# Kernel optimization log

Hardware: AMD Instinct MI355X
Metric: run time of the kernel (lower is better)

Reference implementation:

```python
import jax, jax.numpy as jnp
import numpy as np

B, S, D, H = 4, 2048, 1024, 16
DEPTH = D // H


def setup_inputs() -> dict:
    key = jax.random.key(0)
    ks = jax.random.split(key, 12)
    inp = {
        "Q": jax.random.normal(ks[0], (B, S, D), jnp.float32),
        "K": jax.random.normal(ks[1], (B, S, D), jnp.float32),
        "V": jax.random.normal(ks[2], (B, S, D), jnp.float32),
        "mask": jax.random.randint(ks[3], (B, 1, S, S), 0, 2, jnp.int32),
        "Wq": jax.random.normal(ks[4], (D, D), jnp.float32) / np.sqrt(D),
        "bq": jnp.zeros((D,), jnp.float32),
        "Wk": jax.random.normal(ks[5], (D, D), jnp.float32) / np.sqrt(D),
        "bk": jnp.zeros((D,), jnp.float32),
        "Wv": jax.random.normal(ks[6], (D, D), jnp.float32) / np.sqrt(D),
        "bv": jnp.zeros((D,), jnp.float32),
        "Wo": jax.random.normal(ks[7], (D, D), jnp.float32) / np.sqrt(D),
        "bo": jnp.zeros((D,), jnp.float32),
    }
    return inp


def _split_heads(x):
    # (B, S, D) -> (B, H, S, depth)
    b, s, _ = x.shape
    return x.reshape(b, s, H, DEPTH).transpose(0, 2, 1, 3)


def reference(Q, K, V, mask, Wq, bq, Wk, bk, Wv, bv, Wo, bo):
    q = _split_heads(Q @ Wq + bq)  # (B,H,S,d)
    k = _split_heads(K @ Wk + bk)
    v = _split_heads(V @ Wv + bv)
    scores = jnp.einsum("bhqd,bhkd->bhqk", q, k) / jnp.sqrt(jnp.float32(DEPTH))
    m = mask.astype(jnp.bool_).astype(jnp.float32)  # (B,1,S,S)
    scores = scores + (1.0 - m) * -1e9
    attn = jax.nn.softmax(scores, axis=-1)  # (B,H,S,S)
    ctx = jnp.einsum("bhqk,bhkd->bhqd", attn, v)
    ctx = ctx.transpose(0, 2, 1, 3).reshape(Q.shape[0], -1, D)  # (B,S,D)
    out = ctx @ Wo + bo
    return out, attn
```

## Files before the change

kernel.cpp:

```cpp
#include <hip/hip_runtime.h>
#include <hip/hip_bf16.h>

#define B_ 4
#define S_ 2048
#define D_ 1024
#define H_ 16
#define TSZ 8388608L

typedef short short8 __attribute__((ext_vector_type(8)));
typedef float f32x4 __attribute__((ext_vector_type(4)));

__device__ inline unsigned short f2b(float f) {
  __hip_bfloat16 h = __float2bfloat16(f);
  return __builtin_bit_cast(unsigned short, h);
}
__device__ inline void gld16(const unsigned short* g, unsigned short* l) {
  __builtin_amdgcn_global_load_lds(
      (const __attribute__((address_space(1))) void*)g,
      (__attribute__((address_space(3))) void*)l, 16, 0, 0);
}

__global__ __launch_bounds__(256) void mask_pack(const int* __restrict__ mask,
                                                 unsigned int* __restrict__ mp) {
  long t = (long)blockIdx.x * 256 + threadIdx.x;
  const int4* p = (const int4*)(mask + (t >> 4) * (long)S_ + (t & 15) * 128);
  unsigned int w0 = 0, w1 = 0, w2 = 0, w3 = 0;
#pragma unroll
  for (int c = 0; c < 32; c++) {
    int4 v = p[c];
#pragma unroll
    for (int e = 0; e < 4; e++) {
      int k = c * 4 + e;
      int val = e == 0 ? v.x : e == 1 ? v.y : e == 2 ? v.z : v.w;
      int nb = k >> 4, p16 = k & 15;
      int gg = p16 >> 2, r = p16 & 3;
      unsigned bit = ((unsigned)val & 1u) << (nb * 4 + r);
      if (gg == 0) w0 |= bit; else if (gg == 1) w1 |= bit;
      else if (gg == 2) w2 |= bit; else w3 |= bit;
    }
  }
  *(uint4*)(mp + t * 4) = make_uint4(w0, w1, w2, w3);
}

__global__ __launch_bounds__(256) void cvt3(
    const float* __restrict__ Q, const float* __restrict__ K,
    const float* __restrict__ V, unsigned short* __restrict__ qo,
    unsigned short* __restrict__ ko, unsigned short* __restrict__ vo) {
  int seg = blockIdx.x >> 12;
  long i = ((long)(blockIdx.x & 4095) * 256 + threadIdx.x) * 8;
  const float* in = seg == 0 ? Q : seg == 1 ? K : V;
  unsigned short* out = seg == 0 ? qo : seg == 1 ? ko : vo;
  float4 a = *(const float4*)(in + i);
  float4 b = *(const float4*)(in + i + 4);
  short8 u;
  u[0] = (short)f2b(a.x); u[1] = (short)f2b(a.y);
  u[2] = (short)f2b(a.z); u[3] = (short)f2b(a.w);
  u[4] = (short)f2b(b.x); u[5] = (short)f2b(b.y);
  u[6] = (short)f2b(b.z); u[7] = (short)f2b(b.w);
  *(short8*)(out + i) = u;
}

__global__ __launch_bounds__(256) void transpose_w4(
    const float* __restrict__ W0, const float* __restrict__ W1,
    const float* __restrict__ W2, const float* __restrict__ W3,
    unsigned short* __restrict__ T0, unsigned short* __restrict__ T1,
    unsigned short* __restrict__ T2, unsigned short* __restrict__ T3) {
  __shared__ unsigned short t[64 * 72];
  const int z = blockIdx.z;
  const float* W = z == 0 ? W0 : z == 1 ? W1 : z == 2 ? W2 : W3;
  unsigned short* Wt = z == 0 ? T0 : z == 1 ? T1 : z == 2 ? T2 : T3;
  const int tid = threadIdx.x;
  const int k0 = blockIdx.x * 64, n0 = blockIdx.y * 64;
#pragma unroll
  for (int p = 0; p < 4; p++) {
    int e = (p * 256 + tid) * 4;
    int r = e >> 6, c = e & 63;
    float4 v = *(const float4*)(W + (long)(k0 + r) * D_ + n0 + c);
    ushort4 u;
    u.x = f2b(v.x); u.y = f2b(v.y); u.z = f2b(v.z); u.w = f2b(v.w);
    *(ushort4*)(&t[r * 72 + c]) = u;
  }
  __syncthreads();
#pragma unroll
  for (int p = 0; p < 2; p++) {
    int e = (p * 256 + tid) * 8;
    int n = e >> 6, kc = e & 63;
    short8 x;
#pragma unroll
    for (int i = 0; i < 8; i++) x[i] = (short)t[(kc + i) * 72 + n];
    *(short8*)(Wt + (long)(n0 + n) * D_ + k0 + kc) = x;
  }
}

__global__ __launch_bounds__(256) void qkv_gemm(
    const unsigned short* __restrict__ qa, const unsigned short* __restrict__ ka,
    const unsigned short* __restrict__ va, const unsigned short* __restrict__ wq,
    const unsigned short* __restrict__ wk, const unsigned short* __restrict__ wv,
    const float* __restrict__ bqp, const float* __restrict__ bkp,
    const float* __restrict__ bvp, unsigned short* __restrict__ qo,
    unsigned short* __restrict__ ko, unsigned short* __restrict__ vo) {
  __shared__ unsigned short Asm[128 * 32];
  __shared__ unsigned short Bsm[128 * 32];
  const int z = blockIdx.z;
  const unsigned short* A = z == 0 ? qa : z == 1 ? ka : va;
  const unsigned short* Wt = z == 0 ? wq : z == 1 ? wk : wv;
  const float* bias = z == 0 ? bqp : z == 1 ? bkp : bvp;
  unsigned short* outp = z == 0 ? qo : z == 1 ? ko : vo;
  const int tid = threadIdx.x;
  const int lane = tid & 63, wid = tid >> 6;
  const int g = lane >> 4, li = lane & 15;
  const int wm = wid >> 1, wn = wid & 1;
  const long bm = (long)blockIdx.x * 128;
  const long bn = (long)blockIdx.y * 128;

  f32x4 acc[4][4];
#pragma unroll
  for (int i = 0; i < 4; i++)
#pragma unroll
    for (int j = 0; j < 4; j++) acc[i][j] = (f32x4){0.f, 0.f, 0.f, 0.f};

  for (int kt = 0; kt < 32; ++kt) {
    const int k0 = kt * 32;
    __syncthreads();
#pragma unroll
    for (int p = 0; p < 2; p++) {
      int ci = p * 256 + wid * 64 + lane;
      int r = ci >> 2, c = (ci & 3) * 8;
      gld16(A + (bm + r) * 1024L + k0 + c, &Asm[(p * 256 + wid * 64) * 8]);
      gld16(Wt + (bn + r) * 1024L + k0 + c, &Bsm[(p * 256 + wid * 64) * 8]);
    }
    __syncthreads();
    short8 af[4], bf[4];
#pragma unroll
    for (int i = 0; i < 4; i++)
      af[i] = *(const short8*)(&Asm[(wm * 64 + i * 16 + li) * 32 + g * 8]);
#pragma unroll
    for (int i = 0; i < 4; i++)
      bf[i] = *(const short8*)(&Bsm[(wn * 64 + i * 16 + li) * 32 + g * 8]);
#pragma unroll
    for (int i = 0; i < 4; i++)
#pragma unroll
      for (int j = 0; j < 4; j++)
        acc[i][j] =
            __builtin_amdgcn_mfma_f32_16x16x32_bf16(af[i], bf[j], acc[i][j], 0, 0, 0);
  }

#pragma unroll
  for (int i = 0; i < 4; i++) {
    int row0 = (int)bm + wm * 64 + i * 16 + g * 4;
#pragma unroll
    for (int j = 0; j < 4; j++) {
      int col = (int)bn + wn * 64 + j * 16 + li;
      float bvv = bias[col];
      if (z == 2) {
        int b = row0 >> 11, s0 = row0 & 2047;
        int h = col >> 6, dd = col & 63;
        ushort4 u;
#pragma unroll
        for (int jj = 0; jj < 4; jj++) u[jj] = f2b(acc[i][j][jj] + bvv);
        *(ushort4*)(outp + ((long)(b * H_ + h) * 64 + dd) * S_ + s0) = u;
      } else {
#pragma unroll
        for (int jj = 0; jj < 4; jj++) {
          int row = row0 + jj;
          int b = row >> 11, s = row & 2047;
          int h = col >> 6, dd = col & 63;
          outp[(((long)(b * H_ + h)) * S_ + s) * 64 + dd] =
              f2b(acc[i][j][jj] + bvv);
        }
      }
    }
  }
}

__global__ __launch_bounds__(256) void wo_gemm(
    const unsigned short* __restrict__ A, const unsigned short* __restrict__ Wt,
    const float* __restrict__ bias, float* __restrict__ out) {
  __shared__ unsigned short Asm[128 * 32];
  __shared__ unsigned short Bsm[128 * 32];
  const int tid = threadIdx.x;
  const int lane = tid & 63, wid = tid >> 6;
  const int g = lane >> 4, li = lane & 15;
  const int wm = wid >> 1, wn = wid & 1;
  const long bm = (long)blockIdx.x * 128;
  const long bn = (long)blockIdx.y * 128;

  f32x4 acc[4][4];
#pragma unroll
  for (int i = 0; i < 4; i++)
#pragma unroll
    for (int j = 0; j < 4; j++) acc[i][j] = (f32x4){0.f, 0.f, 0.f, 0.f};

  for (int kt = 0; kt < 32; ++kt) {
    const int k0 = kt * 32;
    __syncthreads();
#pragma unroll
    for (int p = 0; p < 2; p++) {
      int ci = p * 256 + wid * 64 + lane;
      int r = ci >> 2, c = (ci & 3) * 8;
      gld16(A + (bm + r) * 1024L + k0 + c, &Asm[(p * 256 + wid * 64) * 8]);
      gld16(Wt + (bn + r) * 1024L + k0 + c, &Bsm[(p * 256 + wid * 64) * 8]);
    }
    __syncthreads();
    short8 af[4], bf[4];
#pragma unroll
    for (int i = 0; i < 4; i++)
      af[i] = *(const short8*)(&Asm[(wm * 64 + i * 16 + li) * 32 + g * 8]);
#pragma unroll
    for (int i = 0; i < 4; i++)
      bf[i] = *(const short8*)(&Bsm[(wn * 64 + i * 16 + li) * 32 + g * 8]);
#pragma unroll
    for (int i = 0; i < 4; i++)
#pragma unroll
      for (int j = 0; j < 4; j++)
        acc[i][j] =
            __builtin_amdgcn_mfma_f32_16x16x32_bf16(af[i], bf[j], acc[i][j], 0, 0, 0);
  }

#pragma unroll
  for (int i = 0; i < 4; i++) {
    int row0 = (int)bm + wm * 64 + i * 16 + g * 4;
#pragma unroll
    for (int j = 0; j < 4; j++) {
      int col = (int)bn + wn * 64 + j * 16 + li;
      float bvv = bias[col];
#pragma unroll
      for (int jj = 0; jj < 4; jj++)
        out[(long)(row0 + jj) * 1024 + col] = acc[i][j][jj] + bvv;
    }
  }
}

__global__ __launch_bounds__(256, 4) void attn_kernel(
    const unsigned short* __restrict__ q,
    const unsigned short* __restrict__ k,
    const unsigned short* __restrict__ vt,
    const unsigned int* __restrict__ mpk,
    float* __restrict__ attn,
    unsigned short* __restrict__ ctx) {
  __shared__ unsigned short k_lds[128 * 72];
  __shared__ unsigned short vt_lds[64 * 136];
  const int tid = threadIdx.x;
  const int lane = tid & 63, wid = tid >> 6;
  const int g = lane >> 4, li = lane & 15;
  const int p0 = blockIdx.x + 32 * blockIdx.y;
  const int xcd = p0 & 7, q8 = p0 >> 3;
  const int bx = q8 & 31;
  const int bh = xcd * 8 + (q8 >> 5);
  const int b = bh >> 4, h = bh & 15;
  const int qw = bx * 64 + wid * 16;
  const int qs = qw + li;

  const unsigned short* qp = q + ((long)bh * S_ + qw) * 64;
  const short8 aq0 = *(const short8*)(qp + li * 64 + g * 8);
  const short8 aq1 = *(const short8*)(qp + li * 64 + 32 + g * 8);
  const unsigned int* mp = mpk + (((long)b * S_ + qs) * 16) * 4 + g;

  const unsigned short* kbase = k + (long)bh * S_ * 64;
  const unsigned short* vbase = vt + (long)bh * 64 * S_;
  int kst[4], kgo[4], vst[4], vgo[4];
#pragma unroll
  for (int p = 0; p < 4; p++) {
    int e = (p * 256 + tid) * 8;
    int krr = e >> 6, kcc = e & 63;
    kst[p] = krr * 72 + kcc;
    kgo[p] = krr * 64 + kcc;
    int vrr = e >> 7, vcc = e & 127;
    int c0 = ((vcc >> 5) << 5) + ((vcc & 8) << 1) + ((vcc & 16) >> 2);
    vst[p] = vrr * 136 + c0;
    vgo[p] = vrr * S_ + vcc;
  }

  float lsum = 0.f;
  short8 kreg[4];
#pragma unroll
  for (int p = 0; p < 4; p++)
    kreg[p] = *(const short8*)(kbase + kgo[p]);
  unsigned int mb_n = mp[0];
  for (int kt = 0; kt < 16; ++kt) {
    __syncthreads();
#pragma unroll
    for (int p = 0; p < 4; p++)
      *(short8*)(&k_lds[kst[p]]) = kreg[p];
    unsigned int mb = mb_n;
    if (kt < 15) {
#pragma unroll
      for (int p = 0; p < 4; p++)
        kreg[p] = *(const short8*)(kbase + (kt + 1) * 8192 + kgo[p]);
      mb_n = mp[(kt + 1) * 4];
    }
    __syncthreads();
#pragma unroll
    for (int nb = 0; nb < 8; nb++) {
      short8 b0 = *(const short8*)(&k_lds[(nb * 16 + li) * 72 + g * 8]);
      short8 b1 = *(const short8*)(&k_lds[(nb * 16 + li) * 72 + 32 + g * 8]);
      f32x4 s = (f32x4){0.f, 0.f, 0.f, 0.f};
      __builtin_amdgcn_s_setprio(1);
      s = __builtin_amdgcn_mfma_f32_16x16x32_bf16(b0, aq0, s, 0, 0, 0);
      s = __builtin_amdgcn_mfma_f32_16x16x32_bf16(b1, aq1, s, 0, 0, 0);
      __builtin_amdgcn_s_setprio(0);
#pragma unroll
      for (int r = 0; r < 4; r++) {
        float sc = s[r] * 0.125f + (((mb >> (nb * 4 + r)) & 1u) ? 0.f : -1e9f);
        lsum += __expf(sc);
      }
    }
  }
  lsum += __shfl_xor(lsum, 16);
  lsum += __shfl_xor(lsum, 32);
  const float linv = (lsum > 0.f) ? 1.0f / lsum : 0.f;

  f32x4 c[4];
#pragma unroll
  for (int i = 0; i < 4; i++) c[i] = (f32x4){0.f, 0.f, 0.f, 0.f};

  short8 vreg[4];
#pragma unroll
  for (int p = 0; p < 4; p++) {
    kreg[p] = *(const short8*)(kbase + kgo[p]);
    vreg[p] = *(const short8*)(vbase + vgo[p]);
  }
  mb_n = mp[0];
  for (int kt = 0; kt < 16; ++kt) {
    __syncthreads();
#pragma unroll
    for (int p = 0; p < 4; p++) {
      *(short8*)(&k_lds[kst[p]]) = kreg[p];
      ushort4* vh = (ushort4*)&vreg[p];
      *(ushort4*)(&vt_lds[vst[p]]) = vh[0];
      *(ushort4*)(&vt_lds[vst[p] + 8]) = vh[1];
    }
    unsigned int mb = mb_n;
    if (kt < 15) {
#pragma unroll
      for (int p = 0; p < 4; p++) {
        kreg[p] = *(const short8*)(kbase + (kt + 1) * 8192 + kgo[p]);
        vreg[p] = *(const short8*)(vbase + (kt + 1) * 128 + vgo[p]);
      }
      mb_n = mp[(kt + 1) * 4];
    }
    __syncthreads();
    float* arow = attn + ((long)bh * S_ + qs) * S_ + kt * 128;
    short8 pu2[4];
#pragma unroll
    for (int nb = 0; nb < 8; nb++) {
      short8 b0 = *(const short8*)(&k_lds[(nb * 16 + li) * 72 + g * 8]);
      short8 b1 = *(const short8*)(&k_lds[(nb * 16 + li) * 72 + 32 + g * 8]);
      f32x4 s = (f32x4){0.f, 0.f, 0.f, 0.f};
      __builtin_amdgcn_s_setprio(1);
      s = __builtin_amdgcn_mfma_f32_16x16x32_bf16(b0, aq0, s, 0, 0, 0);
      s = __builtin_amdgcn_mfma_f32_16x16x32_bf16(b1, aq1, s, 0, 0, 0);
      __builtin_amdgcn_s_setprio(0);
      f32x4 pf;
      ushort4 pu;
#pragma unroll
      for (int r = 0; r < 4; r++) {
        float sc = s[r] * 0.125f + (((mb >> (nb * 4 + r)) & 1u) ? 0.f : -1e9f);
        float pv = __expf(sc) * linv;
        pf[r] = pv;
        pu[r] = f2b(pv);
      }
      __builtin_nontemporal_store(pf, (f32x4*)(arow + nb * 16 + g * 4));
      ((ushort4*)&pu2[nb >> 1])[nb & 1] = pu;
    }
    __builtin_amdgcn_s_setprio(1);
#pragma unroll
    for (int kc = 0; kc < 4; kc++) {
      short8 ap = pu2[kc];
#pragma unroll
      for (int nb2 = 0; nb2 < 4; nb2++) {
        short8 bv =
            *(const short8*)(&vt_lds[(nb2 * 16 + li) * 136 + kc * 32 + g * 8]);
        c[nb2] = __builtin_amdgcn_mfma_f32_16x16x32_bf16(ap, bv, c[nb2], 0, 0, 0);
      }
    }
    __builtin_amdgcn_s_setprio(0);
  }

#pragma unroll
  for (int nb2 = 0; nb2 < 4; nb2++) {
#pragma unroll
    for (int j = 0; j < 4; j++) {
      int qrow = qw + g * 4 + j;
      ctx[((long)(b * S_ + qrow)) * D_ + h * 64 + nb2 * 16 + li] = f2b(c[nb2][j]);
    }
  }
}

extern "C" void kernel_launch(void* const* d_in, const int* in_sizes, int n_in,
                              void* d_out, int out_size, void* d_ws, size_t ws_size,
                              hipStream_t stream) {
  const float* Q = (const float*)d_in[0];
  const float* K = (const float*)d_in[1];
  const float* V = (const float*)d_in[2];
  const int* mask = (const int*)d_in[3];
  const float* Wq = (const float*)d_in[4];
  const float* bq = (const float*)d_in[5];
  const float* Wk = (const float*)d_in[6];
  const float* bk = (const float*)d_in[7];
  const float* Wv = (const float*)d_in[8];
  const float* bv = (const float*)d_in[9];
  const float* Wo = (const float*)d_in[10];
  const float* bo = (const float*)d_in[11];

  float* out = (float*)d_out;
  float* attn = out + TSZ;
  unsigned int* mpack = (unsigned int*)d_out;

  unsigned short* ws = (unsigned short*)d_ws;
  unsigned short* qh = ws;
  unsigned short* kh = ws + TSZ;
  unsigned short* vt = ws + 2 * TSZ;
  unsigned short* ctx = ws + 3 * TSZ;
  unsigned short* qbf = ws + 4 * TSZ;
  unsigned short* kbf = ws + 5 * TSZ;
  unsigned short* vbf = ws + 6 * TSZ;
  unsigned short* wtq = ws + 7 * TSZ;
  unsigned short* wtk = wtq + 1048576;
  unsigned short* wtv = wtk + 1048576;
  unsigned short* wto = wtv + 1048576;

  dim3 bb(256);
  mask_pack<<<512, bb, 0, stream>>>(mask, mpack);
  cvt3<<<12288, bb, 0, stream>>>(Q, K, V, qbf, kbf, vbf);
  transpose_w4<<<dim3(16, 16, 4), bb, 0, stream>>>(Wq, Wk, Wv, Wo, wtq, wtk,
                                                   wtv, wto);
  qkv_gemm<<<dim3(64, 8, 3), bb, 0, stream>>>(qbf, kbf, vbf, wtq, wtk, wtv, bq,
                                              bk, bv, qh, kh, vt);
  attn_kernel<<<dim3(32, 64), bb, 0, stream>>>(qh, kh, vt, mpack, attn, ctx);
  wo_gemm<<<dim3(64, 8), bb, 0, stream>>>(ctx, wto, bo, out);
}
```

Measured before the change: 476.7 us.

## Process 32 query rows per wave and load V directly into swizzled LDS

Each wave in the attention kernel now handles two 16-row query blocks, so every K and V fragment read from LDS feeds twice as many MFMAs. Each block covers 128 queries and the grid is halved. The V-transpose store in the QKV GEMM is permuted and XOR-swizzled so V tiles can go straight to LDS with global_load_lds, dropping the register staging and the padded layout. Register use grows, so the occupancy hint drops from 4 to 3 blocks per CU.

```diff
diff --git a/kernel.cpp b/kernel.cpp
--- a/kernel.cpp
+++ b/kernel.cpp
@@ -158,7 +158,10 @@
         ushort4 u;
 #pragma unroll
         for (int jj = 0; jj < 4; jj++) u[jj] = f2b(acc[i][j][jj] + bvv);
-        *(ushort4*)(outp + ((long)(b * H_ + h) * 64 + dd) * S_ + s0) = u;
+        int kh2 = s0 & 31;
+        int s1 = (s0 & ~31) | (((kh2 >> 2) & 3) << 3) | (((kh2 >> 4) & 1) << 2);
+        int s2 = s1 ^ ((dd & 7) << 3);
+        *(ushort4*)(outp + ((long)(b * H_ + h) * 64 + dd) * S_ + s2) = u;
       } else {
 #pragma unroll
         for (int jj = 0; jj < 4; jj++) {
@@ -231,7 +234,7 @@
   }
 }
 
-__global__ __launch_bounds__(256, 4) void attn_kernel(
+__global__ __launch_bounds__(256, 3) void attn_kernel(
     const unsigned short* __restrict__ q,
     const unsigned short* __restrict__ k,
     const unsigned short* __restrict__ vt,
@@ -239,152 +242,160 @@
     float* __restrict__ attn,
     unsigned short* __restrict__ ctx) {
   __shared__ unsigned short k_lds[128 * 72];
-  __shared__ unsigned short vt_lds[64 * 136];
+  __shared__ unsigned short v_lds[64 * 128];
   const int tid = threadIdx.x;
-  const int lane = tid & 63, wid = tid >> 6;
+  const int lane = tid & 63, w = tid >> 6;
   const int g = lane >> 4, li = lane & 15;
-  const int p0 = blockIdx.x + 32 * blockIdx.y;
+  const int p0 = blockIdx.x + 16 * blockIdx.y;
   const int xcd = p0 & 7, q8 = p0 >> 3;
-  const int bx = q8 & 31;
-  const int bh = xcd * 8 + (q8 >> 5);
+  const int bx = q8 & 15, bh = xcd * 8 + (q8 >> 4);
   const int b = bh >> 4, h = bh & 15;
-  const int qw = bx * 64 + wid * 16;
-  const int qs = qw + li;
+  const int qw = bx * 128 + w * 32;
 
   const unsigned short* qp = q + ((long)bh * S_ + qw) * 64;
-  const short8 aq0 = *(const short8*)(qp + li * 64 + g * 8);
-  const short8 aq1 = *(const short8*)(qp + li * 64 + 32 + g * 8);
-  const unsigned int* mp = mpk + (((long)b * S_ + qs) * 16) * 4 + g;
+  short8 aq0[2], aq1[2];
+#pragma unroll
+  for (int qb = 0; qb < 2; qb++) {
+    aq0[qb] = *(const short8*)(qp + (qb * 16 + li) * 64 + g * 8);
+    aq1[qb] = *(const short8*)(qp + (qb * 16 + li) * 64 + 32 + g * 8);
+  }
+  const unsigned int* mpb0 = mpk + ((long)(b * S_ + qw + li) * 16) * 4 + g;
+  const unsigned int* mpb1 = mpb0 + 1024;
 
   const unsigned short* kbase = k + (long)bh * S_ * 64;
   const unsigned short* vbase = vt + (long)bh * 64 * S_;
-  int kst[4], kgo[4], vst[4], vgo[4];
+  int kst[4], kgo[4], vsrc[4];
 #pragma unroll
   for (int p = 0; p < 4; p++) {
     int e = (p * 256 + tid) * 8;
-    int krr = e >> 6, kcc = e & 63;
-    kst[p] = krr * 72 + kcc;
-    kgo[p] = krr * 64 + kcc;
-    int vrr = e >> 7, vcc = e & 127;
-    int c0 = ((vcc >> 5) << 5) + ((vcc & 8) << 1) + ((vcc & 16) >> 2);
-    vst[p] = vrr * 136 + c0;
-    vgo[p] = vrr * S_ + vcc;
-  }
-
-  float lsum = 0.f;
+    int kr = e >> 6, kc = e & 63;
+    kst[p] = kr * 72 + kc;
+    kgo[p] = kr * 64 + kc;
+    int ci = p * 256 + tid;
+    vsrc[p] = (ci >> 4) * S_ + (ci & 15) * 8;
+  }
+
+  float ls0 = 0.f, ls1 = 0.f;
   short8 kreg[4];
 #pragma unroll
-  for (int p = 0; p < 4; p++)
-    kreg[p] = *(const short8*)(kbase + kgo[p]);
-  unsigned int mb_n = mp[0];
+  for (int p = 0; p < 4; p++) kreg[p] = *(const short8*)(kbase + kgo[p]);
+  unsigned int mA0 = mpb0[0], mA1 = mpb1[0];
   for (int kt = 0; kt < 16; ++kt) {
     __syncthreads();
 #pragma unroll
-    for (int p = 0; p < 4; p++)
-      *(short8*)(&k_lds[kst[p]]) = kreg[p];
-    unsigned int mb = mb_n;
+    for (int p = 0; p < 4; p++) *(short8*)(&k_lds[kst[p]]) = kreg[p];
+    unsigned int mb0 = mA0, mb1 = mA1;
     if (kt < 15) {
 #pragma unroll
       for (int p = 0; p < 4; p++)
         kreg[p] = *(const short8*)(kbase + (kt + 1) * 8192 + kgo[p]);
-      mb_n = mp[(kt + 1) * 4];
+      mA0 = mpb0[(kt + 1) * 4];
+      mA1 = mpb1[(kt + 1) * 4];
     }
     __syncthreads();
 #pragma unroll
     for (int nb = 0; nb < 8; nb++) {
       short8 b0 = *(const short8*)(&k_lds[(nb * 16 + li) * 72 + g * 8]);
       short8 b1 = *(const short8*)(&k_lds[(nb * 16 + li) * 72 + 32 + g * 8]);
-      f32x4 s = (f32x4){0.f, 0.f, 0.f, 0.f};
+      f32x4 s0 = (f32x4){0.f, 0.f, 0.f, 0.f};
+      f32x4 s1 = (f32x4){0.f, 0.f, 0.f, 0.f};
       __builtin_amdgcn_s_setprio(1);
-      s = __builtin_amdgcn_mfma_f32_16x16x32_bf16(b0, aq0, s, 0, 0, 0);
-      s = __builtin_amdgcn_mfma_f32_16x16x32_bf16(b1, aq1, s, 0, 0, 0);
+      s0 = __builtin_amdgcn_mfma_f32_16x16x32_bf16(b0, aq0[0], s0, 0, 0, 0);
+      s0 = __builtin_amdgcn_mfma_f32_16x16x32_bf16(b1, aq1[0], s0, 0, 0, 0);
+      s1 = __builtin_amdgcn_mfma_f32_16x16x32_bf16(b0, aq0[1], s1, 0, 0, 0);
+      s1 = __builtin_amdgcn_mfma_f32_16x16x32_bf16(b1, aq1[1], s1, 0, 0, 0);
       __builtin_amdgcn_s_setprio(0);
 #pragma unroll
       for (int r = 0; r < 4; r++) {
-        float sc = s[r] * 0.125f + (((mb >> (nb * 4 + r)) & 1u) ? 0.f : -1e9f);
-        lsum += __expf(sc);
+        int bi = nb * 4 + r;
+        ls0 += __expf(s0[r] * 0.125f + (((mb0 >> bi) & 1u) ? 0.f : -1e9f));
+        ls1 += __expf(s1[r] * 0.125f + (((mb1 >> bi) & 1u) ? 0.f : -1e9f));
       }
     }
   }
-  lsum += __shfl_xor(lsum, 16);
-  lsum += __shfl_xor(lsum, 32);
-  const float linv = (lsum > 0.f) ? 1.0f / lsum : 0.f;
-
-  f32x4 c[4];
-#pragma unroll
-  for (int i = 0; i < 4; i++) c[i] = (f32x4){0.f, 0.f, 0.f, 0.f};
-
-  short8 vreg[4];
-#pragma unroll
-  for (int p = 0; p < 4; p++) {
-    kreg[p] = *(const short8*)(kbase + kgo[p]);
-    vreg[p] = *(const short8*)(vbase + vgo[p]);
-  }
-  mb_n = mp[0];
+  ls0 += __shfl_xor(ls0, 16); ls0 += __shfl_xor(ls0, 32);
+  ls1 += __shfl_xor(ls1, 16); ls1 += __shfl_xor(ls1, 32);
+  const float linv0 = (ls0 > 0.f) ? 1.0f / ls0 : 0.f;
+  const float linv1 = (ls1 > 0.f) ? 1.0f / ls1 : 0.f;
+
+  f32x4 c[2][4];
+#pragma unroll
+  for (int qb = 0; qb < 2; qb++)
+#pragma unroll
+    for (int d = 0; d < 4; d++) c[qb][d] = (f32x4){0.f, 0.f, 0.f, 0.f};
+#pragma unroll
+  for (int p = 0; p < 4; p++) kreg[p] = *(const short8*)(kbase + kgo[p]);
+  mA0 = mpb0[0]; mA1 = mpb1[0];
+  float* arow0 = attn + ((long)bh * S_ + qw + li) * S_;
   for (int kt = 0; kt < 16; ++kt) {
     __syncthreads();
 #pragma unroll
     for (int p = 0; p < 4; p++) {
       *(short8*)(&k_lds[kst[p]]) = kreg[p];
-      ushort4* vh = (ushort4*)&vreg[p];
-      *(ushort4*)(&vt_lds[vst[p]]) = vh[0];
-      *(ushort4*)(&vt_lds[vst[p] + 8]) = vh[1];
-    }
-    unsigned int mb = mb_n;
+      gld16(vbase + kt * 128 + vsrc[p], &v_lds[(p * 256 + w * 64) * 8]);
+    }
+    unsigned int mb0 = mA0, mb1 = mA1;
     if (kt < 15) {
 #pragma unroll
-      for (int p = 0; p < 4; p++) {
+      for (int p = 0; p < 4; p++)
         kreg[p] = *(const short8*)(kbase + (kt + 1) * 8192 + kgo[p]);
-        vreg[p] = *(const short8*)(vbase + (kt + 1) * 128 + vgo[p]);
-      }
-      mb_n = mp[(kt + 1) * 4];
-    }
-    __syncthreads();
-    float* arow = attn + ((long)bh * S_ + qs) * S_ + kt * 128;
-    short8 pu2[4];
+      mA0 = mpb0[(kt + 1) * 4];
+      mA1 = mpb1[(kt + 1) * 4];
+    }
+    __syncthreads();
+    short8 pu2[2][4];
 #pragma unroll
     for (int nb = 0; nb < 8; nb++) {
       short8 b0 = *(const short8*)(&k_lds[(nb * 16 + li) * 72 + g * 8]);
       short8 b1 = *(const short8*)(&k_lds[(nb * 16 + li) * 72 + 32 + g * 8]);
-      f32x4 s = (f32x4){0.f, 0.f, 0.f, 0.f};
+      f32x4 s0 = (f32x4){0.f, 0.f, 0.f, 0.f};
+      f32x4 s1 = (f32x4){0.f, 0.f, 0.f, 0.f};
       __builtin_amdgcn_s_setprio(1);
-      s = __builtin_amdgcn_mfma_f32_16x16x32_bf16(b0, aq0, s, 0, 0, 0);
-      s = __builtin_amdgcn_mfma_f32_16x16x32_bf16(b1, aq1, s, 0, 0, 0);
+      s0 = __builtin_amdgcn_mfma_f32_16x16x32_bf16(b0, aq0[0], s0, 0, 0, 0);
+      s0 = __builtin_amdgcn_mfma_f32_16x16x32_bf16(b1, aq1[0], s0, 0, 0, 0);
+      s1 = __builtin_amdgcn_mfma_f32_16x16x32_bf16(b0, aq0[1], s1, 0, 0, 0);
+      s1 = __builtin_amdgcn_mfma_f32_16x16x32_bf16(b1, aq1[1], s1, 0, 0, 0);
       __builtin_amdgcn_s_setprio(0);
-      f32x4 pf;
-      ushort4 pu;
+      f32x4 pf0, pf1;
+      ushort4 pu0, pu1;
 #pragma unroll
       for (int r = 0; r < 4; r++) {
-        float sc = s[r] * 0.125f + (((mb >> (nb * 4 + r)) & 1u) ? 0.f : -1e9f);
-        float pv = __expf(sc) * linv;
-        pf[r] = pv;
-        pu[r] = f2b(pv);
+        int bi = nb * 4 + r;
+        float p0f = __expf(s0[r] * 0.125f + (((mb0 >> bi) & 1u) ? 0.f : -1e9f)) * linv0;
+        float p1f = __expf(s1[r] * 0.125f + (((mb1 >> bi) & 1u) ? 0.f : -1e9f)) * linv1;
+        pf0[r] = p0f; pu0[r] = f2b(p0f);
+        pf1[r] = p1f; pu1[r] = f2b(p1f);
       }
-      __builtin_nontemporal_store(pf, (f32x4*)(arow + nb * 16 + g * 4));
-      ((ushort4*)&pu2[nb >> 1])[nb & 1] = pu;
+      long acol = kt * 128 + nb * 16 + g * 4;
+      __builtin_nontemporal_store(pf0, (f32x4*)(arow0 + acol));
+      __builtin_nontemporal_store(pf1, (f32x4*)(arow0 + 16 * S_ + acol));
+      ((ushort4*)&pu2[0][nb >> 1])[nb & 1] = pu0;
+      ((ushort4*)&pu2[1][nb >> 1])[nb & 1] = pu1;
     }
     __builtin_amdgcn_s_setprio(1);
 #pragma unroll
     for (int kc = 0; kc < 4; kc++) {
-      short8 ap = pu2[kc];
-#pragma unroll
-      for (int nb2 = 0; nb2 < 4; nb2++) {
-        short8 bv =
-            *(const short8*)(&vt_lds[(nb2 * 16 + li) * 136 + kc * 32 + g * 8]);
-        c[nb2] = __builtin_amdgcn_mfma_f32_16x16x32_bf16(ap, bv, c[nb2], 0, 0, 0);
+#pragma unroll
+      for (int d = 0; d < 4; d++) {
+        short8 bv = *(const short8*)(&v_lds[(d * 16 + li) * 128 +
+                                            ((kc * 32 + g * 8) ^ ((li & 7) << 3))]);
+        c[0][d] = __builtin_amdgcn_mfma_f32_16x16x32_bf16(pu2[0][kc], bv, c[0][d], 0, 0, 0);
+        c[1][d] = __builtin_amdgcn_mfma_f32_16x16x32_bf16(pu2[1][kc], bv, c[1][d], 0, 0, 0);
       }
     }
     __builtin_amdgcn_s_setprio(0);
   }
 
 #pragma unroll
-  for (int nb2 = 0; nb2 < 4; nb2++) {
-#pragma unroll
-    for (int j = 0; j < 4; j++) {
-      int qrow = qw + g * 4 + j;
-      ctx[((long)(b * S_ + qrow)) * D_ + h * 64 + nb2 * 16 + li] = f2b(c[nb2][j]);
-    }
-  }
+  for (int qb = 0; qb < 2; qb++)
+#pragma unroll
+    for (int d = 0; d < 4; d++)
+#pragma unroll
+      for (int jj = 0; jj < 4; jj++) {
+        int qrow = qw + qb * 16 + g * 4 + jj;
+        ctx[((long)(b * S_ + qrow)) * D_ + h * 64 + d * 16 + li] =
+            f2b(c[qb][d][jj]);
+      }
 }
 
 extern "C" void kernel_launch(void* const* d_in, const int* in_sizes, int n_in,
@@ -427,6 +438,6 @@
                                                    wtv, wto);
   qkv_gemm<<<dim3(64, 8, 3), bb, 0, stream>>>(qbf, kbf, vbf, wtq, wtk, wtv, bq,
                                               bk, bv, qh, kh, vt);
-  attn_kernel<<<dim3(32, 64), bb, 0, stream>>>(qh, kh, vt, mpack, attn, ctx);
+  attn_kernel<<<dim3(16, 64), bb, 0, stream>>>(qh, kh, vt, mpack, attn, ctx);
   wo_gemm<<<dim3(64, 8), bb, 0, stream>>>(ctx, wto, bo, out);
 }
```

Measured after the change: 495.2 us. 1.04x slower.

## Pre-swizzle V^T in GEMM epilogue and load V tiles via global_load_lds

Applied to the files above, without the earlier changes.

The QKV GEMM epilogue now writes V^T with a permuted and XOR-swizzled sequence order, so the attention kernel can copy V tiles straight into LDS with global_load_lds. This replaces the register staging and split 8-byte LDS stores, and reads use an XOR swizzle to avoid bank conflicts. Separately, the mask packing kernel is merged into the fp32-to-bf16 conversion kernel, saving one launch. The direct LDS load has no explicit wait before the barrier, so correctness depends on the compiler inserting a vmcnt wait.

```diff
diff --git a/kernel.cpp b/kernel.cpp
--- a/kernel.cpp
+++ b/kernel.cpp
@@ -20,44 +20,44 @@
       (__attribute__((address_space(3))) void*)l, 16, 0, 0);
 }
 
-__global__ __launch_bounds__(256) void mask_pack(const int* __restrict__ mask,
-                                                 unsigned int* __restrict__ mp) {
-  long t = (long)blockIdx.x * 256 + threadIdx.x;
-  const int4* p = (const int4*)(mask + (t >> 4) * (long)S_ + (t & 15) * 128);
-  unsigned int w0 = 0, w1 = 0, w2 = 0, w3 = 0;
-#pragma unroll
-  for (int c = 0; c < 32; c++) {
-    int4 v = p[c];
-#pragma unroll
-    for (int e = 0; e < 4; e++) {
-      int k = c * 4 + e;
-      int val = e == 0 ? v.x : e == 1 ? v.y : e == 2 ? v.z : v.w;
-      int nb = k >> 4, p16 = k & 15;
-      int gg = p16 >> 2, r = p16 & 3;
-      unsigned bit = ((unsigned)val & 1u) << (nb * 4 + r);
-      if (gg == 0) w0 |= bit; else if (gg == 1) w1 |= bit;
-      else if (gg == 2) w2 |= bit; else w3 |= bit;
-    }
-  }
-  *(uint4*)(mp + t * 4) = make_uint4(w0, w1, w2, w3);
-}
-
-__global__ __launch_bounds__(256) void cvt3(
+__global__ __launch_bounds__(256) void cvt3m(
     const float* __restrict__ Q, const float* __restrict__ K,
-    const float* __restrict__ V, unsigned short* __restrict__ qo,
-    unsigned short* __restrict__ ko, unsigned short* __restrict__ vo) {
-  int seg = blockIdx.x >> 12;
-  long i = ((long)(blockIdx.x & 4095) * 256 + threadIdx.x) * 8;
-  const float* in = seg == 0 ? Q : seg == 1 ? K : V;
-  unsigned short* out = seg == 0 ? qo : seg == 1 ? ko : vo;
-  float4 a = *(const float4*)(in + i);
-  float4 b = *(const float4*)(in + i + 4);
-  short8 u;
-  u[0] = (short)f2b(a.x); u[1] = (short)f2b(a.y);
-  u[2] = (short)f2b(a.z); u[3] = (short)f2b(a.w);
-  u[4] = (short)f2b(b.x); u[5] = (short)f2b(b.y);
-  u[6] = (short)f2b(b.z); u[7] = (short)f2b(b.w);
-  *(short8*)(out + i) = u;
+    const float* __restrict__ V, const int* __restrict__ mask,
+    unsigned short* __restrict__ qo, unsigned short* __restrict__ ko,
+    unsigned short* __restrict__ vo, unsigned int* __restrict__ mp) {
+  if (blockIdx.x < 12288) {
+    int seg = blockIdx.x >> 12;
+    long i = ((long)(blockIdx.x & 4095) * 256 + threadIdx.x) * 8;
+    const float* in = seg == 0 ? Q : seg == 1 ? K : V;
+    unsigned short* out = seg == 0 ? qo : seg == 1 ? ko : vo;
+    float4 a = *(const float4*)(in + i);
+    float4 b = *(const float4*)(in + i + 4);
+    short8 u;
+    u[0] = (short)f2b(a.x); u[1] = (short)f2b(a.y);
+    u[2] = (short)f2b(a.z); u[3] = (short)f2b(a.w);
+    u[4] = (short)f2b(b.x); u[5] = (short)f2b(b.y);
+    u[6] = (short)f2b(b.z); u[7] = (short)f2b(b.w);
+    *(short8*)(out + i) = u;
+  } else {
+    long t = (long)(blockIdx.x - 12288) * 256 + threadIdx.x;
+    const int4* p = (const int4*)(mask + (t >> 4) * (long)S_ + (t & 15) * 128);
+    unsigned int w0 = 0, w1 = 0, w2 = 0, w3 = 0;
+#pragma unroll
+    for (int c = 0; c < 32; c++) {
+      int4 v = p[c];
+#pragma unroll
+      for (int e = 0; e < 4; e++) {
+        int k = c * 4 + e;
+        int val = e == 0 ? v.x : e == 1 ? v.y : e == 2 ? v.z : v.w;
+        int nb = k >> 4, p16 = k & 15;
+        int gg = p16 >> 2, r = p16 & 3;
+        unsigned bit = ((unsigned)val & 1u) << (nb * 4 + r);
+        if (gg == 0) w0 |= bit; else if (gg == 1) w1 |= bit;
+        else if (gg == 2) w2 |= bit; else w3 |= bit;
+      }
+    }
+    *(uint4*)(mp + t * 4) = make_uint4(w0, w1, w2, w3);
+  }
 }
 
 __global__ __launch_bounds__(256) void transpose_w4(
@@ -158,7 +158,10 @@
         ushort4 u;
 #pragma unroll
         for (int jj = 0; jj < 4; jj++) u[jj] = f2b(acc[i][j][jj] + bvv);
-        *(ushort4*)(outp + ((long)(b * H_ + h) * 64 + dd) * S_ + s0) = u;
+        int kh2 = s0 & 31;
+        int s1 = (s0 & ~31) | (((kh2 >> 2) & 3) << 3) | (((kh2 >> 4) & 1) << 2);
+        int s2 = s1 ^ ((dd & 7) << 3);
+        *(ushort4*)(outp + ((long)(b * H_ + h) * 64 + dd) * S_ + s2) = u;
       } else {
 #pragma unroll
         for (int jj = 0; jj < 4; jj++) {
@@ -239,16 +242,16 @@
     float* __restrict__ attn,
     unsigned short* __restrict__ ctx) {
   __shared__ unsigned short k_lds[128 * 72];
-  __shared__ unsigned short vt_lds[64 * 136];
+  __shared__ unsigned short v_lds[64 * 128];
   const int tid = threadIdx.x;
-  const int lane = tid & 63, wid = tid >> 6;
+  const int lane = tid & 63, w = tid >> 6;
   const int g = lane >> 4, li = lane & 15;
   const int p0 = blockIdx.x + 32 * blockIdx.y;
   const int xcd = p0 & 7, q8 = p0 >> 3;
   const int bx = q8 & 31;
   const int bh = xcd * 8 + (q8 >> 5);
   const int b = bh >> 4, h = bh & 15;
-  const int qw = bx * 64 + wid * 16;
+  const int qw = bx * 64 + w * 16;
   const int qs = qw + li;
 
   const unsigned short* qp = q + ((long)bh * S_ + qw) * 64;
@@ -258,30 +261,26 @@
 
   const unsigned short* kbase = k + (long)bh * S_ * 64;
   const unsigned short* vbase = vt + (long)bh * 64 * S_;
-  int kst[4], kgo[4], vst[4], vgo[4];
+  int kst[4], kgo[4], vsrc[4];
 #pragma unroll
   for (int p = 0; p < 4; p++) {
     int e = (p * 256 + tid) * 8;
-    int krr = e >> 6, kcc = e & 63;
-    kst[p] = krr * 72 + kcc;
-    kgo[p] = krr * 64 + kcc;
-    int vrr = e >> 7, vcc = e & 127;
-    int c0 = ((vcc >> 5) << 5) + ((vcc & 8) << 1) + ((vcc & 16) >> 2);
-    vst[p] = vrr * 136 + c0;
-    vgo[p] = vrr * S_ + vcc;
+    int kr = e >> 6, kc = e & 63;
+    kst[p] = kr * 72 + kc;
+    kgo[p] = kr * 64 + kc;
+    int ci = p * 256 + tid;
+    vsrc[p] = (ci >> 4) * S_ + (ci & 15) * 8;
   }
 
   float lsum = 0.f;
   short8 kreg[4];
 #pragma unroll
-  for (int p = 0; p < 4; p++)
-    kreg[p] = *(const short8*)(kbase + kgo[p]);
+  for (int p = 0; p < 4; p++) kreg[p] = *(const short8*)(kbase + kgo[p]);
   unsigned int mb_n = mp[0];
   for (int kt = 0; kt < 16; ++kt) {
     __syncthreads();
 #pragma unroll
-    for (int p = 0; p < 4; p++)
-      *(short8*)(&k_lds[kst[p]]) = kreg[p];
+    for (int p = 0; p < 4; p++) *(short8*)(&k_lds[kst[p]]) = kreg[p];
     unsigned int mb = mb_n;
     if (kt < 15) {
 #pragma unroll
@@ -313,34 +312,25 @@
   f32x4 c[4];
 #pragma unroll
   for (int i = 0; i < 4; i++) c[i] = (f32x4){0.f, 0.f, 0.f, 0.f};
-
-  short8 vreg[4];
-#pragma unroll
-  for (int p = 0; p < 4; p++) {
-    kreg[p] = *(const short8*)(kbase + kgo[p]);
-    vreg[p] = *(const short8*)(vbase + vgo[p]);
-  }
+#pragma unroll
+  for (int p = 0; p < 4; p++) kreg[p] = *(const short8*)(kbase + kgo[p]);
   mb_n = mp[0];
+  float* arow = attn + ((long)bh * S_ + qs) * S_;
   for (int kt = 0; kt < 16; ++kt) {
     __syncthreads();
 #pragma unroll
     for (int p = 0; p < 4; p++) {
       *(short8*)(&k_lds[kst[p]]) = kreg[p];
-      ushort4* vh = (ushort4*)&vreg[p];
-      *(ushort4*)(&vt_lds[vst[p]]) = vh[0];
-      *(ushort4*)(&vt_lds[vst[p] + 8]) = vh[1];
+      gld16(vbase + kt * 128 + vsrc[p], &v_lds[(p * 256 + w * 64) * 8]);
     }
     unsigned int mb = mb_n;
     if (kt < 15) {
 #pragma unroll
-      for (int p = 0; p < 4; p++) {
+      for (int p = 0; p < 4; p++)
         kreg[p] = *(const short8*)(kbase + (kt + 1) * 8192 + kgo[p]);
-        vreg[p] = *(const short8*)(vbase + (kt + 1) * 128 + vgo[p]);
-      }
       mb_n = mp[(kt + 1) * 4];
     }
     __syncthreads();
-    float* arow = attn + ((long)bh * S_ + qs) * S_ + kt * 128;
     short8 pu2[4];
 #pragma unroll
     for (int nb = 0; nb < 8; nb++) {
@@ -360,29 +350,28 @@
         pf[r] = pv;
         pu[r] = f2b(pv);
       }
-      __builtin_nontemporal_store(pf, (f32x4*)(arow + nb * 16 + g * 4));
+      __builtin_nontemporal_store(pf, (f32x4*)(arow + kt * 128 + nb * 16 + g * 4));
       ((ushort4*)&pu2[nb >> 1])[nb & 1] = pu;
     }
     __builtin_amdgcn_s_setprio(1);
 #pragma unroll
     for (int kc = 0; kc < 4; kc++) {
-      short8 ap = pu2[kc];
-#pragma unroll
-      for (int nb2 = 0; nb2 < 4; nb2++) {
-        short8 bv =
-            *(const short8*)(&vt_lds[(nb2 * 16 + li) * 136 + kc * 32 + g * 8]);
-        c[nb2] = __builtin_amdgcn_mfma_f32_16x16x32_bf16(ap, bv, c[nb2], 0, 0, 0);
+#pragma unroll
+      for (int d = 0; d < 4; d++) {
+        short8 bv = *(const short8*)(&v_lds[(d * 16 + li) * 128 +
+                                            ((kc * 32 + g * 8) ^ ((li & 7) << 3))]);
+        c[d] = __builtin_amdgcn_mfma_f32_16x16x32_bf16(pu2[kc], bv, c[d], 0, 0, 0);
       }
     }
     __builtin_amdgcn_s_setprio(0);
   }
 
 #pragma unroll
-  for (int nb2 = 0; nb2 < 4; nb2++) {
-#pragma unroll
-    for (int j = 0; j < 4; j++) {
-      int qrow = qw + g * 4 + j;
-      ctx[((long)(b * S_ + qrow)) * D_ + h * 64 + nb2 * 16 + li] = f2b(c[nb2][j]);
+  for (int d = 0; d < 4; d++) {
+#pragma unroll
+    for (int jj = 0; jj < 4; jj++) {
+      int qrow = qw + g * 4 + jj;
+      ctx[((long)(b * S_ + qrow)) * D_ + h * 64 + d * 16 + li] = f2b(c[d][jj]);
     }
   }
 }
@@ -421,8 +410,7 @@
   unsigned short* wto = wtv + 1048576;
 
   dim3 bb(256);
-  mask_pack<<<512, bb, 0, stream>>>(mask, mpack);
-  cvt3<<<12288, bb, 0, stream>>>(Q, K, V, qbf, kbf, vbf);
+  cvt3m<<<12800, bb, 0, stream>>>(Q, K, V, mask, qbf, kbf, vbf, mpack);
   transpose_w4<<<dim3(16, 16, 4), bb, 0, stream>>>(Wq, Wk, Wv, Wo, wtq, wtk,
                                                    wtv, wto);
   qkv_gemm<<<dim3(64, 8, 3), bb, 0, stream>>>(qbf, kbf, vbf, wtq, wtk, wtv, bq,
```

Result: slower. 499.4 us (+4.7%).

## Split softmax denominator pass into separate kernel with 4x query reuse per K tile

Applied to the files above, without the earlier changes.

Moves the first pass of the attention kernel, which computes the per-row exp-sum, into its own kernel. Each wave there handles 64 queries against the same K tile in LDS, so K loads and LDS staging are amortized over four times more work. The attention kernel then reads the precomputed inverse sums instead of recomputing them. The mask-pack and bf16-convert kernels are also merged into one launch. The cost is an extra kernel launch and a small workspace buffer.

```diff
diff --git a/kernel.cpp b/kernel.cpp
--- a/kernel.cpp
+++ b/kernel.cpp
@@ -20,44 +20,44 @@
       (__attribute__((address_space(3))) void*)l, 16, 0, 0);
 }
 
-__global__ __launch_bounds__(256) void mask_pack(const int* __restrict__ mask,
-                                                 unsigned int* __restrict__ mp) {
-  long t = (long)blockIdx.x * 256 + threadIdx.x;
-  const int4* p = (const int4*)(mask + (t >> 4) * (long)S_ + (t & 15) * 128);
-  unsigned int w0 = 0, w1 = 0, w2 = 0, w3 = 0;
-#pragma unroll
-  for (int c = 0; c < 32; c++) {
-    int4 v = p[c];
-#pragma unroll
-    for (int e = 0; e < 4; e++) {
-      int k = c * 4 + e;
-      int val = e == 0 ? v.x : e == 1 ? v.y : e == 2 ? v.z : v.w;
-      int nb = k >> 4, p16 = k & 15;
-      int gg = p16 >> 2, r = p16 & 3;
-      unsigned bit = ((unsigned)val & 1u) << (nb * 4 + r);
-      if (gg == 0) w0 |= bit; else if (gg == 1) w1 |= bit;
-      else if (gg == 2) w2 |= bit; else w3 |= bit;
-    }
-  }
-  *(uint4*)(mp + t * 4) = make_uint4(w0, w1, w2, w3);
-}
-
-__global__ __launch_bounds__(256) void cvt3(
+__global__ __launch_bounds__(256) void cvt3m(
     const float* __restrict__ Q, const float* __restrict__ K,
-    const float* __restrict__ V, unsigned short* __restrict__ qo,
-    unsigned short* __restrict__ ko, unsigned short* __restrict__ vo) {
-  int seg = blockIdx.x >> 12;
-  long i = ((long)(blockIdx.x & 4095) * 256 + threadIdx.x) * 8;
-  const float* in = seg == 0 ? Q : seg == 1 ? K : V;
-  unsigned short* out = seg == 0 ? qo : seg == 1 ? ko : vo;
-  float4 a = *(const float4*)(in + i);
-  float4 b = *(const float4*)(in + i + 4);
-  short8 u;
-  u[0] = (short)f2b(a.x); u[1] = (short)f2b(a.y);
-  u[2] = (short)f2b(a.z); u[3] = (short)f2b(a.w);
-  u[4] = (short)f2b(b.x); u[5] = (short)f2b(b.y);
-  u[6] = (short)f2b(b.z); u[7] = (short)f2b(b.w);
-  *(short8*)(out + i) = u;
+    const float* __restrict__ V, const int* __restrict__ mask,
+    unsigned short* __restrict__ qo, unsigned short* __restrict__ ko,
+    unsigned short* __restrict__ vo, unsigned int* __restrict__ mp) {
+  if (blockIdx.x < 12288) {
+    int seg = blockIdx.x >> 12;
+    long i = ((long)(blockIdx.x & 4095) * 256 + threadIdx.x) * 8;
+    const float* in = seg == 0 ? Q : seg == 1 ? K : V;
+    unsigned short* out = seg == 0 ? qo : seg == 1 ? ko : vo;
+    float4 a = *(const float4*)(in + i);
+    float4 b = *(const float4*)(in + i + 4);
+    short8 u;
+    u[0] = (short)f2b(a.x); u[1] = (short)f2b(a.y);
+    u[2] = (short)f2b(a.z); u[3] = (short)f2b(a.w);
+    u[4] = (short)f2b(b.x); u[5] = (short)f2b(b.y);
+    u[6] = (short)f2b(b.z); u[7] = (short)f2b(b.w);
+    *(short8*)(out + i) = u;
+  } else {
+    long t = (long)(blockIdx.x - 12288) * 256 + threadIdx.x;
+    const int4* p = (const int4*)(mask + (t >> 4) * (long)S_ + (t & 15) * 128);
+    unsigned int w0 = 0, w1 = 0, w2 = 0, w3 = 0;
+#pragma unroll
+    for (int c = 0; c < 32; c++) {
+      int4 v = p[c];
+#pragma unroll
+      for (int e = 0; e < 4; e++) {
+        int k = c * 4 + e;
+        int val = e == 0 ? v.x : e == 1 ? v.y : e == 2 ? v.z : v.w;
+        int nb = k >> 4, p16 = k & 15;
+        int gg = p16 >> 2, r = p16 & 3;
+        unsigned bit = ((unsigned)val & 1u) << (nb * 4 + r);
+        if (gg == 0) w0 |= bit; else if (gg == 1) w1 |= bit;
+        else if (gg == 2) w2 |= bit; else w3 |= bit;
+      }
+    }
+    *(uint4*)(mp + t * 4) = make_uint4(w0, w1, w2, w3);
+  }
 }
 
 __global__ __launch_bounds__(256) void transpose_w4(
@@ -231,11 +231,107 @@
   }
 }
 
+__global__ __launch_bounds__(256, 2) void lsum_kernel(
+    const unsigned short* __restrict__ q,
+    const unsigned short* __restrict__ k,
+    const unsigned int* __restrict__ mpk,
+    float* __restrict__ linvb) {
+  __shared__ unsigned short k_lds[128 * 72];
+  const int tid = threadIdx.x;
+  const int lane = tid & 63, w = tid >> 6;
+  const int g = lane >> 4, li = lane & 15;
+  const int p0 = blockIdx.x + 8 * blockIdx.y;
+  const int xcd = p0 & 7, q8 = p0 >> 3;
+  const int bx = q8 & 7, bh = xcd * 8 + (q8 >> 3);
+  const int b = bh >> 4;
+  const int qbase = bx * 256 + w * 64;
+
+  const unsigned short* qp = q + ((long)bh * S_ + qbase) * 64;
+  short8 aq0[4], aq1[4];
+#pragma unroll
+  for (int qb = 0; qb < 4; qb++) {
+    aq0[qb] = *(const short8*)(qp + (qb * 16 + li) * 64 + g * 8);
+    aq1[qb] = *(const short8*)(qp + (qb * 16 + li) * 64 + 32 + g * 8);
+  }
+  const unsigned int* mpb = mpk + ((long)(b * S_ + qbase + li) * 16) * 4 + g;
+
+  const unsigned short* kbase = k + (long)bh * S_ * 64;
+  int kst[4], kgo[4];
+#pragma unroll
+  for (int p = 0; p < 4; p++) {
+    int e = (p * 256 + tid) * 8;
+    int kr = e >> 6, kc = e & 63;
+    kst[p] = kr * 72 + kc;
+    kgo[p] = kr * 64 + kc;
+  }
+
+  float lsum[4] = {0.f, 0.f, 0.f, 0.f};
+  short8 kreg[4];
+#pragma unroll
+  for (int p = 0; p < 4; p++) kreg[p] = *(const short8*)(kbase + kgo[p]);
+  unsigned int mbn[4];
+#pragma unroll
+  for (int qb = 0; qb < 4; qb++) mbn[qb] = mpb[qb * 1024];
+
+  for (int kt = 0; kt < 16; ++kt) {
+    __syncthreads();
+#pragma unroll
+    for (int p = 0; p < 4; p++) *(short8*)(&k_lds[kst[p]]) = kreg[p];
+    unsigned int mb[4];
+#pragma unroll
+    for (int qb = 0; qb < 4; qb++) mb[qb] = mbn[qb];
+    if (kt < 15) {
+#pragma unroll
+      for (int p = 0; p < 4; p++)
+        kreg[p] = *(const short8*)(kbase + (kt + 1) * 8192 + kgo[p]);
+#pragma unroll
+      for (int qb = 0; qb < 4; qb++) mbn[qb] = mpb[qb * 1024 + (kt + 1) * 4];
+    }
+    __syncthreads();
+#pragma unroll
+    for (int nb = 0; nb < 8; nb++) {
+      short8 b0 = *(const short8*)(&k_lds[(nb * 16 + li) * 72 + g * 8]);
+      short8 b1 = *(const short8*)(&k_lds[(nb * 16 + li) * 72 + 32 + g * 8]);
+      f32x4 s0 = (f32x4){0.f, 0.f, 0.f, 0.f};
+      f32x4 s1 = (f32x4){0.f, 0.f, 0.f, 0.f};
+      f32x4 s2 = (f32x4){0.f, 0.f, 0.f, 0.f};
+      f32x4 s3 = (f32x4){0.f, 0.f, 0.f, 0.f};
+      __builtin_amdgcn_s_setprio(1);
+      s0 = __builtin_amdgcn_mfma_f32_16x16x32_bf16(b0, aq0[0], s0, 0, 0, 0);
+      s0 = __builtin_amdgcn_mfma_f32_16x16x32_bf16(b1, aq1[0], s0, 0, 0, 0);
+      s1 = __builtin_amdgcn_mfma_f32_16x16x32_bf16(b0, aq0[1], s1, 0, 0, 0);
+      s1 = __builtin_amdgcn_mfma_f32_16x16x32_bf16(b1, aq1[1], s1, 0, 0, 0);
+      s2 = __builtin_amdgcn_mfma_f32_16x16x32_bf16(b0, aq0[2], s2, 0, 0, 0);
+      s2 = __builtin_amdgcn_mfma_f32_16x16x32_bf16(b1, aq1[2], s2, 0, 0, 0);
+      s3 = __builtin_amdgcn_mfma_f32_16x16x32_bf16(b0, aq0[3], s3, 0, 0, 0);
+      s3 = __builtin_amdgcn_mfma_f32_16x16x32_bf16(b1, aq1[3], s3, 0, 0, 0);
+      __builtin_amdgcn_s_setprio(0);
+#pragma unroll
+      for (int r = 0; r < 4; r++) {
+        int bi = nb * 4 + r;
+        lsum[0] += __expf(s0[r] * 0.125f + (((mb[0] >> bi) & 1u) ? 0.f : -1e9f));
+        lsum[1] += __expf(s1[r] * 0.125f + (((mb[1] >> bi) & 1u) ? 0.f : -1e9f));
+        lsum[2] += __expf(s2[r] * 0.125f + (((mb[2] >> bi) & 1u) ? 0.f : -1e9f));
+        lsum[3] += __expf(s3[r] * 0.125f + (((mb[3] >> bi) & 1u) ? 0.f : -1e9f));
+      }
+    }
+  }
+#pragma unroll
+  for (int qb = 0; qb < 4; qb++) {
+    float v = lsum[qb];
+    v += __shfl_xor(v, 16);
+    v += __shfl_xor(v, 32);
+    if (lane < 16)
+      linvb[(long)bh * S_ + qbase + qb * 16 + li] = (v > 0.f) ? 1.0f / v : 0.f;
+  }
+}
+
 __global__ __launch_bounds__(256, 4) void attn_kernel(
     const unsigned short* __restrict__ q,
     const unsigned short* __restrict__ k,
     const unsigned short* __restrict__ vt,
     const unsigned int* __restrict__ mpk,
+    const float* __restrict__ linvb,
     float* __restrict__ attn,
     unsigned short* __restrict__ ctx) {
   __shared__ unsigned short k_lds[128 * 72];
@@ -255,6 +351,7 @@
   const short8 aq0 = *(const short8*)(qp + li * 64 + g * 8);
   const short8 aq1 = *(const short8*)(qp + li * 64 + 32 + g * 8);
   const unsigned int* mp = mpk + (((long)b * S_ + qs) * 16) * 4 + g;
+  const float linv = linvb[(long)bh * S_ + qs];
 
   const unsigned short* kbase = k + (long)bh * S_ * 64;
   const unsigned short* vbase = vt + (long)bh * 64 * S_;
@@ -271,56 +368,17 @@
     vgo[p] = vrr * S_ + vcc;
   }
 
-  float lsum = 0.f;
-  short8 kreg[4];
-#pragma unroll
-  for (int p = 0; p < 4; p++)
-    kreg[p] = *(const short8*)(kbase + kgo[p]);
-  unsigned int mb_n = mp[0];
-  for (int kt = 0; kt < 16; ++kt) {
-    __syncthreads();
-#pragma unroll
-    for (int p = 0; p < 4; p++)
-      *(short8*)(&k_lds[kst[p]]) = kreg[p];
-    unsigned int mb = mb_n;
-    if (kt < 15) {
-#pragma unroll
-      for (int p = 0; p < 4; p++)
-        kreg[p] = *(const short8*)(kbase + (kt + 1) * 8192 + kgo[p]);
-      mb_n = mp[(kt + 1) * 4];
-    }
-    __syncthreads();
-#pragma unroll
-    for (int nb = 0; nb < 8; nb++) {
-      short8 b0 = *(const short8*)(&k_lds[(nb * 16 + li) * 72 + g * 8]);
-      short8 b1 = *(const short8*)(&k_lds[(nb * 16 + li) * 72 + 32 + g * 8]);
-      f32x4 s = (f32x4){0.f, 0.f, 0.f, 0.f};
-      __builtin_amdgcn_s_setprio(1);
-      s = __builtin_amdgcn_mfma_f32_16x16x32_bf16(b0, aq0, s, 0, 0, 0);
-      s = __builtin_amdgcn_mfma_f32_16x16x32_bf16(b1, aq1, s, 0, 0, 0);
-      __builtin_amdgcn_s_setprio(0);
-#pragma unroll
-      for (int r = 0; r < 4; r++) {
-        float sc = s[r] * 0.125f + (((mb >> (nb * 4 + r)) & 1u) ? 0.f : -1e9f);
-        lsum += __expf(sc);
-      }
-    }
-  }
-  lsum += __shfl_xor(lsum, 16);
-  lsum += __shfl_xor(lsum, 32);
-  const float linv = (lsum > 0.f) ? 1.0f / lsum : 0.f;
-
   f32x4 c[4];
 #pragma unroll
   for (int i = 0; i < 4; i++) c[i] = (f32x4){0.f, 0.f, 0.f, 0.f};
 
-  short8 vreg[4];
+  short8 kreg[4], vreg[4];
 #pragma unroll
   for (int p = 0; p < 4; p++) {
     kreg[p] = *(const short8*)(kbase + kgo[p]);
     vreg[p] = *(const short8*)(vbase + vgo[p]);
   }
-  mb_n = mp[0];
+  unsigned int mb_n = mp[0];
   for (int kt = 0; kt < 16; ++kt) {
     __syncthreads();
 #pragma unroll
@@ -419,14 +477,16 @@
   unsigned short* wtk = wtq + 1048576;
   unsigned short* wtv = wtk + 1048576;
   unsigned short* wto = wtv + 1048576;
+  float* linvb = (float*)(wto + 1048576);
 
   dim3 bb(256);
-  mask_pack<<<512, bb, 0, stream>>>(mask, mpack);
-  cvt3<<<12288, bb, 0, stream>>>(Q, K, V, qbf, kbf, vbf);
+  cvt3m<<<12800, bb, 0, stream>>>(Q, K, V, mask, qbf, kbf, vbf, mpack);
   transpose_w4<<<dim3(16, 16, 4), bb, 0, stream>>>(Wq, Wk, Wv, Wo, wtq, wtk,
                                                    wtv, wto);
   qkv_gemm<<<dim3(64, 8, 3), bb, 0, stream>>>(qbf, kbf, vbf, wtq, wtk, wtv, bq,
                                               bk, bv, qh, kh, vt);
-  attn_kernel<<<dim3(32, 64), bb, 0, stream>>>(qh, kh, vt, mpack, attn, ctx);
+  lsum_kernel<<<dim3(8, 64), bb, 0, stream>>>(qh, kh, mpack, linvb);
+  attn_kernel<<<dim3(32, 64), bb, 0, stream>>>(qh, kh, vt, mpack, linvb, attn,
+                                               ctx);
   wo_gemm<<<dim3(64, 8), bb, 0, stream>>>(ctx, wto, bo, out);
 }
```

Result: slower. 562.1 us (+17.9%).
